# Performance work log

Hardware: AMD Instinct MI355X
Metric: run time of the kernel (lower is better)

The kernel has to match this reference:

```python
import jax, jax.numpy as jnp
import numpy as np

NUM_BRANCHES = 4
REP_DIM = 1024
FEAT_DIM = 128
N_DATA = 100000
NCE_K = 4096
NCE_T = 0.07
BATCH = 128
EPS = 1e-07


def setup_inputs() -> dict:
    key = jax.random.key(0)
    ks = jax.random.split(key, 8)
    d = {}
    for i in range(NUM_BRANCHES):
        d[f"emb{i}"] = jax.random.normal(ks[i], (BATCH, REP_DIM), dtype=jnp.float32)
    d["W"] = jax.random.normal(ks[4], (NUM_BRANCHES, FEAT_DIM, REP_DIM), dtype=jnp.float32) * 0.03
    d["b"] = jnp.zeros((NUM_BRANCHES, FEAT_DIM), dtype=jnp.float32)
    stdv = 1.0 / np.sqrt(FEAT_DIM / 3.0)
    d["memory"] = jax.random.uniform(ks[5], (NUM_BRANCHES, N_DATA, FEAT_DIM), dtype=jnp.float32, minval=-stdv, maxval=stdv)
    idx = jax.random.randint(ks[6], (BATCH,), 0, N_DATA)
    neg = jax.random.randint(ks[7], (BATCH, NCE_K), 0, N_DATA)
    d["idx"] = idx
    d["contrast_idx"] = jnp.concatenate([idx[:, None], neg], axis=1)  # col 0 = positive
    return d


def reference(emb0, emb1, emb2, emb3, W, b, memory, idx, contrast_idx):
    # per-branch Embed: flatten -> Linear -> L2 normalize
    embs = jnp.stack([emb0, emb1, emb2, emb3], axis=0)            # [R,B,rep]
    h = jnp.einsum('rbi,rdi->rbd', embs, W) + b[:, None, :]        # [R,B,D]
    e = h / jnp.sqrt(jnp.sum(h * h, axis=-1, keepdims=True))       # Normalize(power=2)

    # ContrastMemory: gather K+1 bank rows per sample per branch (detached)
    w = jax.lax.stop_gradient(memory[:, contrast_idx, :])          # [R,B,K+1,D]
    # scores[i,j,b,k] = <bank_j row, emb_i>  for every ordered pair
    scores = jnp.einsum('jbkd,ibd->ijbk', w, e)                    # [R,R,B,K+1]
    out = jnp.exp(scores / NCE_T)
    Z = jax.lax.stop_gradient(jnp.mean(out, axis=(2, 3)) * N_DATA)  # per-pair Z estimate
    out = out / Z[:, :, None, None]

    # ContrastLoss (Eq 11)
    m = float(NCE_K)
    Pn = 1.0 / float(N_DATA)
    pos = out[:, :, :, 0]                                          # [R,R,B]
    neg = out[:, :, :, 1:]                                         # [R,R,B,K]
    log_D1 = jnp.log(pos / (pos + m * Pn + EPS))
    log_D0 = jnp.log((m * Pn) / (neg + m * Pn + EPS))
    per_pair = -(jnp.sum(log_D1, axis=2) + jnp.sum(log_D0, axis=(2, 3))) / BATCH
    mask = 1.0 - jnp.eye(NUM_BRANCHES, dtype=per_pair.dtype)       # only i != j pairs
    return jnp.sum(per_pair * mask)
```

## Files before the change

kernel.cpp:

```cpp
#include <hip/hip_runtime.h>
#include <math.h>

#define NBR    4
#define REP    1024
#define FD     128
#define NDATA  100000
#define KP1    4097
#define BN     128
#define MPN    0.04096f
#define EPS_C  1e-7f
#define TINV   (1.0f / 0.07f)
#define NSLOT  64

typedef unsigned int   uint4e   __attribute__((ext_vector_type(4)));
typedef unsigned short ushort4e __attribute__((ext_vector_type(4)));
typedef _Float16       half2e   __attribute__((ext_vector_type(2)));

static __device__ __forceinline__ unsigned short f2h(float f) {
    union { _Float16 h; unsigned short u; } c; c.h = (_Float16)f; return c.u;
}
static __device__ __forceinline__ float h_lo(unsigned int u) {
    union { unsigned int u; _Float16 h[2]; } c; c.u = u; return (float)c.h[0];
}
static __device__ __forceinline__ float h_hi(unsigned int u) {
    union { unsigned int u; _Float16 h[2]; } c; c.u = u; return (float)c.h[1];
}
static __device__ __forceinline__ half2e u2h2(unsigned int u) {
    union { unsigned int u; half2e h; } c; c.u = u; return c.h;
}
static __device__ __forceinline__ unsigned short f2bf(float f) {
    union { float f; unsigned int u; } c; c.f = f;
    unsigned int u = c.u;
    u += 0x7fffu + ((u >> 16) & 1u);
    return (unsigned short)(u >> 16);
}
static __device__ __forceinline__ float bf2f(unsigned short h) {
    union { unsigned int u; float f; } c; c.u = ((unsigned int)h) << 16;
    return c.f;
}

__global__ void k_convert_t(const float* __restrict__ src, ushort* __restrict__ dst) {
    const size_t t = (size_t)blockIdx.x * 256 + threadIdx.x;
    const size_t total = (size_t)NBR * NDATA * 32;
    if (t >= total) return;
    unsigned int jn = (unsigned int)(t >> 5);
    unsigned int q  = (unsigned int)(t & 31);
    unsigned int j  = jn / (unsigned int)NDATA;
    unsigned int n  = jn - j * (unsigned int)NDATA;
    uint4e v = __builtin_nontemporal_load((const uint4e*)src + t);
    union { unsigned int u; float f; } c0, c1, c2, c3;
    c0.u = v.x; c1.u = v.y; c2.u = v.z; c3.u = v.w;
    ushort4e o;
    o.x = f2h(c0.f); o.y = f2h(c1.f); o.z = f2h(c2.f); o.w = f2h(c3.f);
    ((ushort4e*)dst)[((size_t)n * NBR + j) * 32 + q] = o;
}

__global__ void k_feat(const float* __restrict__ e0, const float* __restrict__ e1,
                       const float* __restrict__ e2, const float* __restrict__ e3,
                       const float* __restrict__ W, const float* __restrict__ bias,
                       float* __restrict__ e_out) {
    const int r = blockIdx.x;
    const int b = blockIdx.y;
    const float* emb = (r == 0 ? e0 : r == 1 ? e1 : r == 2 ? e2 : e3) + (size_t)b * REP;

    __shared__ float s_emb[REP];
    for (int i = threadIdx.x; i < REP; i += blockDim.x) s_emb[i] = emb[i];
    __syncthreads();

    const int d = threadIdx.x;
    const float4* wrow = (const float4*)(W + ((size_t)r * FD + d) * REP);
    float acc = 0.f;
#pragma unroll 8
    for (int c = 0; c < REP / 4; ++c) {
        float4 v = wrow[c];
        acc += v.x * s_emb[4*c+0] + v.y * s_emb[4*c+1]
             + v.z * s_emb[4*c+2] + v.w * s_emb[4*c+3];
    }
    float h = acc + bias[r * FD + d];

    __shared__ float red[FD];
    red[d] = h * h;
    __syncthreads();
    for (int off = FD / 2; off > 0; off >>= 1) {
        if (d < off) red[d] += red[d + off];
        __syncthreads();
    }
    float nrm = sqrtf(red[0]);
    e_out[((size_t)r * BN + b) * FD + d] = h / nrm;
}

__global__ __launch_bounds__(256)
void k_pass1w(const float* __restrict__ e, const ushort* __restrict__ memT,
              const int* __restrict__ cidx, float* __restrict__ Zsl,
              ushort* __restrict__ expS) {
    const int b    = blockIdx.y;
    const int lane = threadIdx.x & 63;
    const int w    = threadIdx.x >> 6;
    const int wid  = w + (blockIdx.x << 2);
    const int nw   = gridDim.x << 2;
    const int l4   = lane & 15;
    const int d0   = l4 * 8;
    const bool b3  = (l4 & 8) != 0;
    const bool b2  = (l4 & 4) != 0;

    half2e eh[4][4];
#pragma unroll
    for (int i = 0; i < 4; ++i) {
        const float4* ep = (const float4*)(e + ((size_t)i * BN + b) * FD + d0);
        float4 v0 = ep[0], v1 = ep[1];
        eh[i][0] = half2e{(_Float16)v0.x, (_Float16)v0.y};
        eh[i][1] = half2e{(_Float16)v0.z, (_Float16)v0.w};
        eh[i][2] = half2e{(_Float16)v1.x, (_Float16)v1.y};
        eh[i][3] = half2e{(_Float16)v1.z, (_Float16)v1.w};
    }

    const int*   ci  = cidx + (size_t)b * KP1;
    const uint4* mt  = (const uint4*)memT;
    ushort*      esb = expS + (size_t)b * (KP1 * 16);

    float z = 0.f;

    int k = wid;
    uint4 A, B;
    if (k < KP1)      A = mt[(size_t)ci[k] * 64 + lane];
    if (k + nw < KP1) B = mt[(size_t)ci[k + nw] * 64 + lane];

    for (; k < KP1; k += nw) {
        uint4 cur = A;
        A = B;
        const int kpf = k + 2 * nw;
        if (kpf < KP1) B = mt[(size_t)ci[kpf] * 64 + lane];

        float a0 = 0.f, a1 = 0.f, a2 = 0.f, a3 = 0.f;
#pragma unroll
        for (int q = 0; q < 4; ++q) {
            half2e hw = u2h2((&cur.x)[q]);
            a0 = __builtin_amdgcn_fdot2(hw, eh[0][q], a0, false);
            a1 = __builtin_amdgcn_fdot2(hw, eh[1][q], a1, false);
            a2 = __builtin_amdgcn_fdot2(hw, eh[2][q], a2, false);
            a3 = __builtin_amdgcn_fdot2(hw, eh[3][q], a3, false);
        }
        float t0 = __shfl_xor(b3 ? a0 : a2, 8, 64);
        float t1 = __shfl_xor(b3 ? a1 : a3, 8, 64);
        float c0 = (b3 ? a2 : a0) + t0;
        float c1 = (b3 ? a3 : a1) + t1;
        float t2 = __shfl_xor(b2 ? c0 : c1, 4, 64);
        float d  = (b2 ? c1 : c0) + t2;
        d += __shfl_xor(d, 2, 64);
        d += __shfl_xor(d, 1, 64);
        float x = __expf(d * TINV);
        z += x;
        if ((lane & 3) == 0)
            esb[(size_t)k * 16 + (lane >> 2)] = f2h(x);
    }

    __shared__ float s_z[4][16];
    const int j = lane >> 4;
    const int i = ((l4 >> 3) << 1) | ((l4 >> 2) & 1);
    if ((lane & 3) == 0) s_z[w][i * 4 + j] = z;
    __syncthreads();
    if (threadIdx.x < 16) {
        float v = s_z[0][threadIdx.x] + s_z[1][threadIdx.x]
                + s_z[2][threadIdx.x] + s_z[3][threadIdx.x];
        const int slot = (blockIdx.y * gridDim.x + blockIdx.x) & (NSLOT - 1);
        atomicAdd(&Zsl[slot * 16 + threadIdx.x], v);
    }
}

__global__ void k_zred(const float* __restrict__ Zsl, float* __restrict__ Zsum) {
    if (threadIdx.x < 16) {
        float s = 0.f;
        for (int sl = 0; sl < NSLOT; ++sl) s += Zsl[sl * 16 + threadIdx.x];
        Zsum[threadIdx.x] = s;
    }
}

static __device__ __forceinline__ void acc_words(const uint4& p0, const uint4& p1,
                                                 const float* __restrict__ s_zinv,
                                                 float* __restrict__ acc, bool pos) {
    unsigned int wds[8] = {p0.x, p0.y, p0.z, p0.w, p1.x, p1.y, p1.z, p1.w};
#pragma unroll
    for (int w = 0; w < 8; ++w) {
        float v0 = h_lo(wds[w]) * s_zinv[2*w];
        float v1 = h_hi(wds[w]) * s_zinv[2*w+1];
        if (pos) {
            acc[2*w]   += -__logf(1.f + (MPN + EPS_C) / v0);
            acc[2*w+1] += -__logf(1.f + (MPN + EPS_C) / v1);
        } else {
            acc[2*w]   += -__logf(1.f + (v0 + EPS_C) * (1.f / MPN));
            acc[2*w+1] += -__logf(1.f + (v1 + EPS_C) * (1.f / MPN));
        }
    }
}

__global__ __launch_bounds__(256)
void k_pass2f(const uint4* __restrict__ expS, const float* __restrict__ Zsum,
              float* __restrict__ Asl) {
    const int b = blockIdx.y;

    __shared__ float s_zinv[16];
    if (threadIdx.x < 16) {
        int jj = threadIdx.x >> 2, ii = threadIdx.x & 3;
        float Z = Zsum[ii * 4 + jj] *
                  (float)((double)NDATA / ((double)BN * (double)KP1));
        s_zinv[threadIdx.x] = 1.0f / Z;
    }
    __syncthreads();

    const uint4* es = expS + (size_t)b * (KP1 * 2);
    const int base = threadIdx.x + blockIdx.x * 256;

    float acc[16];
#pragma unroll
    for (int t = 0; t < 16; ++t) acc[t] = 0.f;

#pragma unroll
    for (int it = 0; it < 2; ++it) {
        const int k = base + it * 2048;
        uint4 p0 = es[(size_t)k * 2];
        uint4 p1 = es[(size_t)k * 2 + 1];
        acc_words(p0, p1, s_zinv, acc, k == 0);
    }
    if (base == 0) {
        uint4 p0 = es[(size_t)4096 * 2];
        uint4 p1 = es[(size_t)4096 * 2 + 1];
        acc_words(p0, p1, s_zinv, acc, false);
    }

#pragma unroll
    for (int t = 0; t < 16; ++t) {
#pragma unroll
        for (int off = 32; off > 0; off >>= 1)
            acc[t] += __shfl_down(acc[t], off, 64);
    }
    __shared__ float s_a[4][16];
    const int w = threadIdx.x >> 6;
    if ((threadIdx.x & 63) == 0) {
#pragma unroll
        for (int t = 0; t < 16; ++t) s_a[w][t] = acc[t];
    }
    __syncthreads();
    if (threadIdx.x < 16) {
        float v = s_a[0][threadIdx.x] + s_a[1][threadIdx.x]
                + s_a[2][threadIdx.x] + s_a[3][threadIdx.x];
        const int slot = (blockIdx.y * gridDim.x + blockIdx.x) & (NSLOT - 1);
        atomicAdd(&Asl[slot * 16 + threadIdx.x], v);
    }
}

__global__ void k_final_slots(const float* __restrict__ Asl, float* __restrict__ out) {
    const int tid = threadIdx.x;
    const int comp = tid & 15;
    const int grp  = tid >> 4;
    float a = 0.f;
    for (int sl = grp; sl < NSLOT; sl += 16) a += Asl[sl * 16 + comp];
    const float m = ((comp >> 2) != (comp & 3)) ? 1.f : 0.f;
    __shared__ float s[256];
    s[tid] = a * m;
    __syncthreads();
    for (int off = 128; off > 0; off >>= 1) {
        if (tid < off) s[tid] += s[tid + off];
        __syncthreads();
    }
    if (tid == 0) out[0] = -s[0] / (float)BN;
}

static __device__ __forceinline__ void dot4(const float4* __restrict__ row,
                                            const float* __restrict__ se,
                                            float& a0, float& a1, float& a2, float& a3) {
    a0 = a1 = a2 = a3 = 0.f;
#pragma unroll 8
    for (int c = 0; c < FD / 4; ++c) {
        float4 v = row[c];
        const int o = 4 * c;
        a0 += v.x * se[0*FD+o+0] + v.y * se[0*FD+o+1] + v.z * se[0*FD+o+2] + v.w * se[0*FD+o+3];
        a1 += v.x * se[1*FD+o+0] + v.y * se[1*FD+o+1] + v.z * se[1*FD+o+2] + v.w * se[1*FD+o+3];
        a2 += v.x * se[2*FD+o+0] + v.y * se[2*FD+o+1] + v.z * se[2*FD+o+2] + v.w * se[2*FD+o+3];
        a3 += v.x * se[3*FD+o+0] + v.y * se[3*FD+o+1] + v.z * se[3*FD+o+2] + v.w * se[3*FD+o+3];
    }
}

static __device__ __forceinline__ void block_reduce4(float z0, float z1, float z2,
                                                     float z3, float* dst, int j) {
    __shared__ float sred[256];
    float zs[NBR] = {z0, z1, z2, z3};
    for (int i = 0; i < NBR; ++i) {
        sred[threadIdx.x] = zs[i];
        __syncthreads();
        for (int off = 128; off > 0; off >>= 1) {
            if ((int)threadIdx.x < off) sred[threadIdx.x] += sred[threadIdx.x + off];
            __syncthreads();
        }
        if (threadIdx.x == 0) atomicAdd(&dst[i * NBR + j], sred[0]);
        __syncthreads();
    }
}

static __device__ __forceinline__ float term_of(float ex, float zinv, int k) {
    const float c = MPN + EPS_C;
    float v = ex * zinv;
    if (k == 0) return -__logf(1.0f + c / v);
    return -__logf(1.0f + (v + EPS_C) * (1.0f / MPN));
}

template <bool STORE>
__global__ void k_pass1_f32(const float* __restrict__ e, const float* __restrict__ memory,
                            const int* __restrict__ cidx,
                            float* __restrict__ Zsum, ushort4* __restrict__ expS) {
    const int j = blockIdx.z;
    const int b = blockIdx.y;

    __shared__ float s_e[NBR * FD];
    for (int t = threadIdx.x; t < NBR * FD; t += blockDim.x) {
        int i = t >> 7, d = t & (FD - 1);
        s_e[t] = e[((size_t)i * BN + b) * FD + d];
    }
    __syncthreads();

    const int* ci = cidx + (size_t)b * KP1;
    const float4* mem4 = (const float4*)(memory + (size_t)j * NDATA * FD);
    float z0 = 0.f, z1 = 0.f, z2 = 0.f, z3 = 0.f;

    for (int k = threadIdx.x + blockIdx.x * blockDim.x; k < KP1;
         k += blockDim.x * gridDim.x) {
        const int n = ci[k];
        const float4* row = mem4 + (size_t)n * (FD / 4);
        float a0, a1, a2, a3;
        dot4(row, s_e, a0, a1, a2, a3);
        float x0 = __expf(a0 * TINV);
        float x1 = __expf(a1 * TINV);
        float x2 = __expf(a2 * TINV);
        float x3 = __expf(a3 * TINV);
        z0 += x0; z1 += x1; z2 += x2; z3 += x3;
        if (STORE) {
            ushort4 st;
            st.x = f2bf(x0); st.y = f2bf(x1); st.z = f2bf(x2); st.w = f2bf(x3);
            expS[((size_t)j * BN + b) * KP1 + k] = st;
        }
    }
    block_reduce4(z0, z1, z2, z3, Zsum, j);
}

__global__ void k_pass2_stored(const ushort4* __restrict__ expS,
                               const float* __restrict__ Zsum,
                               float* __restrict__ accum) {
    const int j = blockIdx.z;
    const int b = blockIdx.y;

    __shared__ float s_zinv[NBR];
    if (threadIdx.x < NBR) {
        float Z = Zsum[threadIdx.x * NBR + j] *
                  (float)((double)NDATA / ((double)BN * (double)KP1));
        s_zinv[threadIdx.x] = 1.0f / Z;
    }
    __syncthreads();

    const ushort4* es = expS + ((size_t)j * BN + b) * KP1;
    float a0 = 0.f, a1 = 0.f, a2 = 0.f, a3 = 0.f;

    for (int k = threadIdx.x + blockIdx.x * blockDim.x; k < KP1;
         k += blockDim.x * gridDim.x) {
        ushort4 v = es[k];
        a0 += term_of(bf2f(v.x), s_zinv[0], k);
        a1 += term_of(bf2f(v.y), s_zinv[1], k);
        a2 += term_of(bf2f(v.z), s_zinv[2], k);
        a3 += term_of(bf2f(v.w), s_zinv[3], k);
    }
    block_reduce4(a0, a1, a2, a3, accum, j);
}

__global__ void k_pass2_regather(const float* __restrict__ e, const float* __restrict__ memory,
                                 const int* __restrict__ cidx,
                                 const float* __restrict__ Zsum, float* __restrict__ accum) {
    const int j = blockIdx.z;
    const int b = blockIdx.y;

    __shared__ float s_e[NBR * FD];
    __shared__ float s_zinv[NBR];
    for (int t = threadIdx.x; t < NBR * FD; t += blockDim.x) {
        int i = t >> 7, d = t & (FD - 1);
        s_e[t] = e[((size_t)i * BN + b) * FD + d];
    }
    if (threadIdx.x < NBR) {
        float Z = Zsum[threadIdx.x * NBR + j] *
                  (float)((double)NDATA / ((double)BN * (double)KP1));
        s_zinv[threadIdx.x] = 1.0f / Z;
    }
    __syncthreads();

    const int* ci = cidx + (size_t)b * KP1;
    const float4* mem4 = (const float4*)(memory + (size_t)j * NDATA * FD);
    float a0s = 0.f, a1s = 0.f, a2s = 0.f, a3s = 0.f;

    for (int k = threadIdx.x + blockIdx.x * blockDim.x; k < KP1;
         k += blockDim.x * gridDim.x) {
        const int n = ci[k];
        const float4* row = mem4 + (size_t)n * (FD / 4);
        float a0, a1, a2, a3;
        dot4(row, s_e, a0, a1, a2, a3);
        a0s += term_of(__expf(a0 * TINV), s_zinv[0], k);
        a1s += term_of(__expf(a1 * TINV), s_zinv[1], k);
        a2s += term_of(__expf(a2 * TINV), s_zinv[2], k);
        a3s += term_of(__expf(a3 * TINV), s_zinv[3], k);
    }
    block_reduce4(a0s, a1s, a2s, a3s, accum, j);
}

__global__ void k_init(float* __restrict__ p, int n) {
    int i = blockIdx.x * blockDim.x + threadIdx.x;
    if (i < n) p[i] = 0.f;
}

__global__ void k_final_legacy(const float* __restrict__ accum, float* __restrict__ out) {
    if (threadIdx.x == 0) {
        float s = 0.f;
        for (int i = 0; i < NBR; ++i)
            for (int j = 0; j < NBR; ++j)
                if (i != j) s += -accum[i * NBR + j] / (float)BN;
        out[0] = s;
    }
}

extern "C" void kernel_launch(void* const* d_in, const int* in_sizes, int n_in,
                              void* d_out, int out_size, void* d_ws, size_t ws_size,
                              hipStream_t stream) {
    const float* e0   = (const float*)d_in[0];
    const float* e1   = (const float*)d_in[1];
    const float* e2   = (const float*)d_in[2];
    const float* e3   = (const float*)d_in[3];
    const float* W    = (const float*)d_in[4];
    const float* bias = (const float*)d_in[5];
    const float* mem  = (const float*)d_in[6];
    const int*   cidx = (const int*)d_in[8];
    float* out = (float*)d_out;

    float* ws    = (float*)d_ws;
    float* e     = ws;
    float* Zsum  = ws + 65536;
    float* accum = ws + 65552;
    float* Zsl   = ws + 65568;
    float* Asl   = ws + 66592;
    const size_t base_b = (size_t)67616 * 4;
    const size_t memT_b = (size_t)NDATA * NBR * FD * 2;
    const size_t expS_b = (size_t)BN * KP1 * 16 * 2;

    const size_t need_full = base_b + memT_b + expS_b;
    const size_t need_mid  = base_b + expS_b;

    k_init<<<9, 256, 0, stream>>>(Zsum, 2080);
    k_feat<<<dim3(NBR, BN), 128, 0, stream>>>(e0, e1, e2, e3, W, bias, e);

    if (ws_size >= need_full) {
        ushort* memT = (ushort*)((char*)d_ws + base_b);
        ushort* expS = (ushort*)((char*)d_ws + base_b + memT_b);
        k_convert_t<<<50000, 256, 0, stream>>>(mem, memT);
        k_pass1w<<<dim3(16, BN), 256, 0, stream>>>(e, memT, cidx, Zsl, expS);
        k_zred<<<1, 64, 0, stream>>>(Zsl, Zsum);
        k_pass2f<<<dim3(8, BN), 256, 0, stream>>>((const uint4*)expS, Zsum, Asl);
        k_final_slots<<<1, 256, 0, stream>>>(Asl, out);
    } else if (ws_size >= need_mid) {
        ushort4* expS = (ushort4*)((char*)d_ws + base_b);
        k_pass1_f32<true><<<dim3(4, BN, NBR), 256, 0, stream>>>(e, mem, cidx, Zsum, expS);
        k_pass2_stored<<<dim3(4, BN, NBR), 256, 0, stream>>>(expS, Zsum, accum);
        k_final_legacy<<<1, 64, 0, stream>>>(accum, out);
    } else {
        k_pass1_f32<false><<<dim3(4, BN, NBR), 256, 0, stream>>>(e, mem, cidx, Zsum, nullptr);
        k_pass2_regather<<<dim3(4, BN, NBR), 256, 0, stream>>>(e, mem, cidx, Zsum, accum);
        k_final_legacy<<<1, 64, 0, stream>>>(accum, out);
    }
}
```

Measured before the change: 427.1 us.

## Replace full memory-bank fp16 conversion with sorted inverse-index gather

Drops the kernel that converted and transposed the whole 4x100000x128 fp32 memory bank to fp16 on every call. It builds an inverse index instead (histogram, prefix scan, scatter) that groups all (b,k) references by bank row. The pass-1 kernel then walks those groups, loads each referenced fp32 row once, and reuses it across repeated references, reading the per-sample embeddings from a new fp16 copy. This removes about 200MB of conversion traffic at the cost of atomics, three extra small kernels, scattered expS writes and less coalesced fp32 row reads.

```diff
diff --git a/kernel.cpp b/kernel.cpp
--- a/kernel.cpp
+++ b/kernel.cpp
@@ -11,10 +11,13 @@
 #define EPS_C  1e-7f
 #define TINV   (1.0f / 0.07f)
 #define NSLOT  64
+#define TREFS  (BN * KP1)
+#define NWAVE  8192
 
 typedef unsigned int   uint4e   __attribute__((ext_vector_type(4)));
 typedef unsigned short ushort4e __attribute__((ext_vector_type(4)));
 typedef _Float16       half2e   __attribute__((ext_vector_type(2)));
+typedef float          floatx4  __attribute__((ext_vector_type(4)));
 
 static __device__ __forceinline__ unsigned short f2h(float f) {
     union { _Float16 h; unsigned short u; } c; c.h = (_Float16)f; return c.u;
@@ -39,26 +42,10 @@
     return c.f;
 }
 
-__global__ void k_convert_t(const float* __restrict__ src, ushort* __restrict__ dst) {
-    const size_t t = (size_t)blockIdx.x * 256 + threadIdx.x;
-    const size_t total = (size_t)NBR * NDATA * 32;
-    if (t >= total) return;
-    unsigned int jn = (unsigned int)(t >> 5);
-    unsigned int q  = (unsigned int)(t & 31);
-    unsigned int j  = jn / (unsigned int)NDATA;
-    unsigned int n  = jn - j * (unsigned int)NDATA;
-    uint4e v = __builtin_nontemporal_load((const uint4e*)src + t);
-    union { unsigned int u; float f; } c0, c1, c2, c3;
-    c0.u = v.x; c1.u = v.y; c2.u = v.z; c3.u = v.w;
-    ushort4e o;
-    o.x = f2h(c0.f); o.y = f2h(c1.f); o.z = f2h(c2.f); o.w = f2h(c3.f);
-    ((ushort4e*)dst)[((size_t)n * NBR + j) * 32 + q] = o;
-}
-
 __global__ void k_feat(const float* __restrict__ e0, const float* __restrict__ e1,
                        const float* __restrict__ e2, const float* __restrict__ e3,
                        const float* __restrict__ W, const float* __restrict__ bias,
-                       float* __restrict__ e_out) {
+                       float* __restrict__ e_out, ushort* __restrict__ eh16) {
     const int r = blockIdx.x;
     const int b = blockIdx.y;
     const float* emb = (r == 0 ? e0 : r == 1 ? e1 : r == 2 ? e2 : e3) + (size_t)b * REP;
@@ -86,59 +73,111 @@
         __syncthreads();
     }
     float nrm = sqrtf(red[0]);
-    e_out[((size_t)r * BN + b) * FD + d] = h / nrm;
+    float val = h / nrm;
+    e_out[((size_t)r * BN + b) * FD + d] = val;
+    if (eh16) eh16[((size_t)r * BN + b) * FD + d] = f2h(val);
+}
+
+__global__ void k_hist(const int* __restrict__ cidx, int* __restrict__ counts) {
+    const int k = blockIdx.x * 256 + threadIdx.x;
+    if (k >= KP1) return;
+    const int b = blockIdx.y;
+    atomicAdd(&counts[cidx[(size_t)b * KP1 + k]], 1);
+}
+
+__global__ void k_assign(const int* __restrict__ counts, int* __restrict__ start,
+                         int* __restrict__ cursor) {
+    __shared__ int s[256];
+    __shared__ int sbase;
+    const int tid = threadIdx.x;
+    const int n = blockIdx.x * 256 + tid;
+    int c = (n < NDATA) ? counts[n] : 0;
+    s[tid] = c;
+    __syncthreads();
+#pragma unroll
+    for (int off = 1; off < 256; off <<= 1) {
+        int v = (tid >= off) ? s[tid - off] : 0;
+        __syncthreads();
+        s[tid] += v;
+        __syncthreads();
+    }
+    if (tid == 255) sbase = atomicAdd(cursor, s[255]);
+    __syncthreads();
+    if (n < NDATA) start[n] = sbase + s[tid] - c;
+}
+
+__global__ void k_scatter(const int* __restrict__ cidx, const int* __restrict__ start,
+                          int* __restrict__ fill, unsigned long long* __restrict__ inv64) {
+    const int k = blockIdx.x * 256 + threadIdx.x;
+    if (k >= KP1) return;
+    const int b = blockIdx.y;
+    const int n = cidx[(size_t)b * KP1 + k];
+    const int pos = atomicAdd(&fill[n], 1);
+    inv64[(size_t)start[n] + pos] =
+        ((unsigned long long)(unsigned int)n << 20) |
+        ((unsigned long long)(unsigned int)b << 13) |
+        (unsigned long long)(unsigned int)k;
 }
 
 __global__ __launch_bounds__(256)
-void k_pass1w(const float* __restrict__ e, const ushort* __restrict__ memT,
-              const int* __restrict__ cidx, float* __restrict__ Zsl,
-              ushort* __restrict__ expS) {
-    const int b    = blockIdx.y;
+void k_pass1i(const float* __restrict__ mem, const ushort* __restrict__ eh16,
+              const unsigned long long* __restrict__ inv64,
+              float* __restrict__ Zsl, ushort* __restrict__ expS) {
     const int lane = threadIdx.x & 63;
     const int w    = threadIdx.x >> 6;
-    const int wid  = w + (blockIdx.x << 2);
-    const int nw   = gridDim.x << 2;
+    const int g    = (blockIdx.x << 2) + w;
     const int l4   = lane & 15;
+    const int jj   = lane >> 4;
     const int d0   = l4 * 8;
     const bool b3  = (l4 & 8) != 0;
     const bool b2  = (l4 & 4) != 0;
 
-    half2e eh[4][4];
-#pragma unroll
-    for (int i = 0; i < 4; ++i) {
-        const float4* ep = (const float4*)(e + ((size_t)i * BN + b) * FD + d0);
-        float4 v0 = ep[0], v1 = ep[1];
-        eh[i][0] = half2e{(_Float16)v0.x, (_Float16)v0.y};
-        eh[i][1] = half2e{(_Float16)v0.z, (_Float16)v0.w};
-        eh[i][2] = half2e{(_Float16)v1.x, (_Float16)v1.y};
-        eh[i][3] = half2e{(_Float16)v1.z, (_Float16)v1.w};
-    }
-
-    const int*   ci  = cidx + (size_t)b * KP1;
-    const uint4* mt  = (const uint4*)memT;
-    ushort*      esb = expS + (size_t)b * (KP1 * 16);
+    const int base = g * 64 + (g < 128 ? g : 128);
+    const int end  = base + 64 + (g < 128 ? 1 : 0);
+
+    const float* mrow_base = mem + (size_t)jj * NDATA * FD + d0;
+    const ushort* eb_base  = eh16 + d0;
 
     float z = 0.f;
-
-    int k = wid;
-    uint4 A, B;
-    if (k < KP1)      A = mt[(size_t)ci[k] * 64 + lane];
-    if (k + nw < KP1) B = mt[(size_t)ci[k + nw] * 64 + lane];
-
-    for (; k < KP1; k += nw) {
-        uint4 cur = A;
-        A = B;
-        const int kpf = k + 2 * nw;
-        if (kpf < KP1) B = mt[(size_t)ci[kpf] * 64 + lane];
+    int n_prev = -1;
+    half2e mh[4];
+    mh[0] = half2e{(_Float16)0.f, (_Float16)0.f};
+    mh[1] = mh[0]; mh[2] = mh[0]; mh[3] = mh[0];
+
+    unsigned long long vnext = inv64[base];
+    for (int c = base; c < end; ++c) {
+        const unsigned long long v = vnext;
+        if (c + 1 < end) vnext = inv64[c + 1];
+        const int n = (int)(v >> 20);
+        const unsigned int bk = (unsigned int)v & 0xFFFFFu;
+        const int b = (int)(bk >> 13);
+        const int k = (int)(bk & 8191u);
+
+        const ushort* eb = eb_base + (size_t)b * FD;
+        uint4 ev0 = *(const uint4*)(eb);
+        uint4 ev1 = *(const uint4*)(eb + (size_t)1 * BN * FD);
+        uint4 ev2 = *(const uint4*)(eb + (size_t)2 * BN * FD);
+        uint4 ev3 = *(const uint4*)(eb + (size_t)3 * BN * FD);
+
+        if (n != n_prev) {
+            const floatx4* mp = (const floatx4*)(mrow_base + (size_t)n * FD);
+            floatx4 v0 = __builtin_nontemporal_load(mp);
+            floatx4 v1 = __builtin_nontemporal_load(mp + 1);
+            mh[0] = half2e{(_Float16)v0.x, (_Float16)v0.y};
+            mh[1] = half2e{(_Float16)v0.z, (_Float16)v0.w};
+            mh[2] = half2e{(_Float16)v1.x, (_Float16)v1.y};
+            mh[3] = half2e{(_Float16)v1.z, (_Float16)v1.w};
+            n_prev = n;
+        }
 
         float a0 = 0.f, a1 = 0.f, a2 = 0.f, a3 = 0.f;
 #pragma unroll
         for (int q = 0; q < 4; ++q) {
-            half2e hw = u2h2((&cur.x)[q]);
-            a0 = __builtin_amdgcn_fdot2(hw, eh[0][q], a0, false);
-            a1 = __builtin_amdgcn_fdot2(hw, eh[1][q], a1, false);
-            a2 = __builtin_amdgcn_fdot2(hw, eh[2][q], a2, false);
-            a3 = __builtin_amdgcn_fdot2(hw, eh[3][q], a3, false);
+            half2e hw = mh[q];
+            a0 = __builtin_amdgcn_fdot2(hw, u2h2((&ev0.x)[q]), a0, false);
+            a1 = __builtin_amdgcn_fdot2(hw, u2h2((&ev1.x)[q]), a1, false);
+            a2 = __builtin_amdgcn_fdot2(hw, u2h2((&ev2.x)[q]), a2, false);
+            a3 = __builtin_amdgcn_fdot2(hw, u2h2((&ev3.x)[q]), a3, false);
         }
         float t0 = __shfl_xor(b3 ? a0 : a2, 8, 64);
         float t1 = __shfl_xor(b3 ? a1 : a3, 8, 64);
@@ -151,19 +190,18 @@
         float x = __expf(d * TINV);
         z += x;
         if ((lane & 3) == 0)
-            esb[(size_t)k * 16 + (lane >> 2)] = f2h(x);
+            expS[((size_t)b * KP1 + k) * 16 + (lane >> 2)] = f2h(x);
     }
 
     __shared__ float s_z[4][16];
-    const int j = lane >> 4;
     const int i = ((l4 >> 3) << 1) | ((l4 >> 2) & 1);
-    if ((lane & 3) == 0) s_z[w][i * 4 + j] = z;
+    if ((lane & 3) == 0) s_z[w][i * 4 + jj] = z;
     __syncthreads();
     if (threadIdx.x < 16) {
-        float v = s_z[0][threadIdx.x] + s_z[1][threadIdx.x]
-                + s_z[2][threadIdx.x] + s_z[3][threadIdx.x];
-        const int slot = (blockIdx.y * gridDim.x + blockIdx.x) & (NSLOT - 1);
-        atomicAdd(&Zsl[slot * 16 + threadIdx.x], v);
+        float vv = s_z[0][threadIdx.x] + s_z[1][threadIdx.x]
+                 + s_z[2][threadIdx.x] + s_z[3][threadIdx.x];
+        const int slot = blockIdx.x & (NSLOT - 1);
+        atomicAdd(&Zsl[slot * 16 + threadIdx.x], vv);
     }
 }
 
@@ -440,30 +478,53 @@
     float* accum = ws + 65552;
     float* Zsl   = ws + 65568;
     float* Asl   = ws + 66592;
-    const size_t base_b = (size_t)67616 * 4;
-    const size_t memT_b = (size_t)NDATA * NBR * FD * 2;
-    const size_t expS_b = (size_t)BN * KP1 * 16 * 2;
-
-    const size_t need_full = base_b + memT_b + expS_b;
+    const size_t base_b   = (size_t)67616 * 4;
+    const size_t eh16_b   = (size_t)NBR * BN * FD * 2;
+    const size_t cnt_b    = (size_t)NDATA * 4;
+    const size_t cur_b    = 16;
+    const size_t inv_b    = (size_t)TREFS * 8;
+    const size_t expS_b   = (size_t)BN * KP1 * 16 * 2;
+
+    const size_t off_eh16   = base_b;
+    const size_t off_counts = off_eh16 + eh16_b;
+    const size_t off_fill   = off_counts + cnt_b;
+    const size_t off_cursor = off_fill + cnt_b;
+    const size_t off_start  = off_cursor + cur_b;
+    const size_t off_inv    = off_start + cnt_b;
+    const size_t off_expS   = off_inv + inv_b;
+
+    const size_t need_full = off_expS + expS_b;
     const size_t need_mid  = base_b + expS_b;
 
-    k_init<<<9, 256, 0, stream>>>(Zsum, 2080);
-    k_feat<<<dim3(NBR, BN), 128, 0, stream>>>(e0, e1, e2, e3, W, bias, e);
-
     if (ws_size >= need_full) {
-        ushort* memT = (ushort*)((char*)d_ws + base_b);
-        ushort* expS = (ushort*)((char*)d_ws + base_b + memT_b);
-        k_convert_t<<<50000, 256, 0, stream>>>(mem, memT);
-        k_pass1w<<<dim3(16, BN), 256, 0, stream>>>(e, memT, cidx, Zsl, expS);
+        ushort* eh16 = (ushort*)((char*)d_ws + off_eh16);
+        int* counts  = (int*)((char*)d_ws + off_counts);
+        int* fill    = (int*)((char*)d_ws + off_fill);
+        int* cursor  = (int*)((char*)d_ws + off_cursor);
+        int* start   = (int*)((char*)d_ws + off_start);
+        unsigned long long* inv64 = (unsigned long long*)((char*)d_ws + off_inv);
+        ushort* expS = (ushort*)((char*)d_ws + off_expS);
+
+        k_init<<<9, 256, 0, stream>>>(Zsum, 2080);
+        k_init<<<782, 256, 0, stream>>>((float*)counts, 200004);
+        k_feat<<<dim3(NBR, BN), 128, 0, stream>>>(e0, e1, e2, e3, W, bias, e, eh16);
+        k_hist<<<dim3(17, BN), 256, 0, stream>>>(cidx, counts);
+        k_assign<<<391, 256, 0, stream>>>(counts, start, cursor);
+        k_scatter<<<dim3(17, BN), 256, 0, stream>>>(cidx, start, fill, inv64);
+        k_pass1i<<<2048, 256, 0, stream>>>(mem, eh16, inv64, Zsl, expS);
         k_zred<<<1, 64, 0, stream>>>(Zsl, Zsum);
         k_pass2f<<<dim3(8, BN), 256, 0, stream>>>((const uint4*)expS, Zsum, Asl);
         k_final_slots<<<1, 256, 0, stream>>>(Asl, out);
     } else if (ws_size >= need_mid) {
+        k_init<<<9, 256, 0, stream>>>(Zsum, 2080);
+        k_feat<<<dim3(NBR, BN), 128, 0, stream>>>(e0, e1, e2, e3, W, bias, e, nullptr);
         ushort4* expS = (ushort4*)((char*)d_ws + base_b);
         k_pass1_f32<true><<<dim3(4, BN, NBR), 256, 0, stream>>>(e, mem, cidx, Zsum, expS);
         k_pass2_stored<<<dim3(4, BN, NBR), 256, 0, stream>>>(expS, Zsum, accum);
         k_final_legacy<<<1, 64, 0, stream>>>(accum, out);
     } else {
+        k_init<<<9, 256, 0, stream>>>(Zsum, 2080);
+        k_feat<<<dim3(NBR, BN), 128, 0, stream>>>(e0, e1, e2, e3, W, bias, e, nullptr);
         k_pass1_f32<false><<<dim3(4, BN, NBR), 256, 0, stream>>>(e, mem, cidx, Zsum, nullptr);
         k_pass2_regather<<<dim3(4, BN, NBR), 256, 0, stream>>>(e, mem, cidx, Zsum, accum);
         k_final_legacy<<<1, 64, 0, stream>>>(accum, out);
```

Result: slower. 484.2 us (+13.4%).
